# Kernel tuning notes

Measured on AMD Instinct MI355X. Metric: run time of the kernel, lower is better.

The kernel has to match this reference:

```python
import jax, jax.numpy as jnp
import numpy as np

N = 400_000   # active voxels
C = 128       # inplanes = outplanes
K = 9         # nplanes*3*3 kernel offsets (nplanes=1)
EPS = 1e-4    # scn BatchNormalization default eps


def setup_inputs() -> dict:
    key = jax.random.key(0)
    ks = jax.random.split(key, 5)
    feat = jax.random.normal(ks[0], (N, C), dtype=jnp.float32)
    # rulebook: neighbor active-site index per kernel offset, plus validity mask
    nbr_idx = jax.random.randint(ks[1], (N, K), 0, N, dtype=jnp.int32)
    nbr_idx = nbr_idx.at[:, K // 2].set(jnp.arange(N, dtype=jnp.int32))  # center = self
    nbr_mask = jax.random.uniform(ks[2], (N, K)) < 0.6
    nbr_mask = nbr_mask.at[:, K // 2].set(True)
    scale = 1.0 / np.sqrt(K * C)
    W1 = jax.random.normal(ks[3], (K, C, C), dtype=jnp.float32) * scale
    W2 = jax.random.normal(ks[4], (K, C, C), dtype=jnp.float32) * scale
    gamma1 = jnp.ones((C,), jnp.float32)
    beta1 = jnp.zeros((C,), jnp.float32)
    gamma2 = jnp.ones((C,), jnp.float32)
    beta2 = jnp.zeros((C,), jnp.float32)
    return {"feat": feat, "W1": W1, "W2": W2,
            "gamma1": gamma1, "beta1": beta1,
            "gamma2": gamma2, "beta2": beta2,
            "nbr_idx": nbr_idx, "nbr_mask": nbr_mask}


def _subm_conv(feat, nbr_idx, nbr_mask, W):
    # rulebook gather -> GEMM -> accumulate; output lives at the same active sites
    out = jnp.zeros((feat.shape[0], W.shape[2]), feat.dtype)
    for k in range(W.shape[0]):  # small fixed K=9 structural loop
        xk = jnp.where(nbr_mask[:, k:k + 1], feat[nbr_idx[:, k]], 0.0)
        out = out + xk @ W[k]
    return out


def _batchnorm(x, gamma, beta):
    mu = jnp.mean(x, axis=0)
    var = jnp.mean(jnp.square(x - mu), axis=0)
    return (x - mu) * (gamma * jax.lax.rsqrt(var + EPS)) + beta


def reference(feat, W1, W2, gamma1, beta1, gamma2, beta2, nbr_idx, nbr_mask):
    residual = feat                                   # scn.Identity (stride=1)
    out = _subm_conv(feat, nbr_idx, nbr_mask, W1)     # conv1
    out = jax.nn.relu(_batchnorm(out, gamma1, beta1))  # BatchNormReLU
    out = _subm_conv(out, nbr_idx, nbr_mask, W2)      # conv2
    out = _batchnorm(out, gamma2, beta2)              # bn2
    return jax.nn.relu(out + residual)                # AddTable + ReLU
```

## Files before the change

kernel.cpp:

```cpp
#include <hip/hip_runtime.h>


#define C_CH 128
#define K_OFF 9
#define MTILE 64

typedef __attribute__((ext_vector_type(8))) short bf16x8;
typedef __attribute__((ext_vector_type(4))) float f32x4;
typedef __attribute__((ext_vector_type(8))) unsigned short u16x8;

typedef __attribute__((address_space(1))) const unsigned int* gas_p;
typedef __attribute__((address_space(3))) unsigned int* las_p;

__device__ __forceinline__ void gload_lds16(const unsigned short* g, unsigned short* l) {
    __builtin_amdgcn_global_load_lds((gas_p)g, (las_p)l, 16, 0, 0);
}

__device__ __forceinline__ unsigned short f2b(float f) {
    union { float f; unsigned u; } v; v.f = f;
    unsigned r = v.u + 0x7fffu + ((v.u >> 16) & 1u);
    return (unsigned short)(r >> 16);
}
__device__ __forceinline__ float b2f(unsigned short h) {
    union { unsigned u; float f; } v; v.u = ((unsigned)h) << 16;
    return v.f;
}


__global__ void init_k(float* stats, unsigned int* zrow1, unsigned int* zrow2) {
    int t = threadIdx.x;
    if (t < 512) stats[t] = 0.f;
    if (t >= 512 && t < 514) ((int*)stats)[1024 + (t - 512)] = 0;
    if (t < 64) { zrow1[t] = 0u; zrow2[t] = 0u; }
}

__global__ void detect_mask_k(const unsigned char* __restrict__ m, int* flagA, int* flagB) {
    int i = blockIdx.x * blockDim.x + threadIdx.x;
    unsigned char v = m[i];
    if ((i & 3) != 0 && v != 0) atomicOr(flagA, 1);
    if (v > 1) atomicOr(flagB, 1);
}

__global__ void fold_idx_k(const int* __restrict__ nidx, const void* __restrict__ m,
                           const int* __restrict__ flagA, const int* __restrict__ flagB,
                           int* __restrict__ eidx, int n, int N) {
    int i = blockIdx.x * blockDim.x + threadIdx.x;
    if (i >= n) return;
    int fa = *flagA, fb = *flagB;
    bool t;
    if (!fa)       t = ((const int*)m)[i] != 0;
    else if (fb)   t = ((const unsigned*)m)[i] != 0;
    else           t = ((const unsigned char*)m)[i] != 0;
    eidx[i] = t ? nidx[i] : N;
}

__global__ void convert_feat_k(const float* __restrict__ x, unsigned short* __restrict__ y, int n4) {
    int i = blockIdx.x * blockDim.x + threadIdx.x;
    int s = gridDim.x * blockDim.x;
    for (; i < n4; i += s) {
        float4 f = ((const float4*)x)[i];
        ushort4 o;
        o.x = f2b(f.x); o.y = f2b(f.y); o.z = f2b(f.z); o.w = f2b(f.w);
        ((ushort4*)y)[i] = o;
    }
}

__global__ void pack_w_k(const float* __restrict__ W, unsigned short* __restrict__ Wp) {
    int i = blockIdx.x * blockDim.x + threadIdx.x;
    if (i >= K_OFF * 8 * 4 * 512) return;
    int j = i & 7;
    int l = (i >> 3) & 63;
    int frag = i >> 9;
    int ks = frag & 3;
    int nt = (frag >> 2) & 7;
    int ko = frag >> 5;
    int cin = ks * 32 + (l >> 4) * 8 + j;
    int cout = nt * 16 + (l & 15);
    Wp[i] = f2b(W[ko * C_CH * C_CH + cin * C_CH + cout]);
}


__global__ __launch_bounds__(256) void conv_kernel(
    const unsigned short* __restrict__ Xb,
    const unsigned short* __restrict__ Wp,
    const int* __restrict__ eidx,
    unsigned short* __restrict__ Yraw,
    float* __restrict__ statS, float* __restrict__ statQ)
{
    const int tid = threadIdx.x;
    const int lane = tid & 63;
    const int wv = tid >> 6;
    const int tile = blockIdx.x * MTILE;
    const int asub = lane >> 4;
    const int l15 = lane & 15;

    __shared__ alignas(16) unsigned short At[2][MTILE * C_CH];
    __shared__ int sIdxT[K_OFF][MTILE];

    for (int i = tid; i < MTILE * K_OFF; i += 256) {
        int r = i / K_OFF, k = i - r * K_OFF;
        sIdxT[k][r] = eidx[(size_t)(tile + r) * K_OFF + k];
    }
    __syncthreads();

    const int r_st = tid >> 4;
    const int ch_st = tid & 15;

    #define STAGE(buf, ko)                                                        \
        {                                                                         \
            _Pragma("unroll")                                                     \
            for (int jr = 0; jr < 4; ++jr) {                                      \
                int r = jr * 16 + r_st;                                           \
                int g = sIdxT[ko][r];                                             \
                const unsigned short* src =                                       \
                    Xb + (size_t)g * C_CH + ((ch_st ^ (r & 7)) * 8);              \
                unsigned short* dst = &At[buf][r * C_CH + ch_st * 8];             \
                gload_lds16(src, dst);                                            \
            }                                                                     \
        }

    f32x4 acc[4][2];
    #pragma unroll
    for (int m = 0; m < 4; ++m) { acc[m][0] = (f32x4){0,0,0,0}; acc[m][1] = (f32x4){0,0,0,0}; }

    STAGE(0, 0);
    __syncthreads();

    for (int ko = 0; ko < K_OFF; ++ko) {
        const int cur = ko & 1;

        bf16x8 bfrag[2][4];
        const unsigned short* wb = Wp + (size_t)ko * (8 * 4 * 512) + lane * 8;
        #pragma unroll
        for (int j = 0; j < 2; ++j)
            #pragma unroll
            for (int ks = 0; ks < 4; ++ks)
                bfrag[j][ks] = *(const bf16x8*)(wb + ((wv * 2 + j) * 4 + ks) * 512);

        if (ko < K_OFF - 1) STAGE(cur ^ 1, ko + 1);

        #pragma unroll
        for (int m = 0; m < 4; ++m) {
            bf16x8 a[4];
            #pragma unroll
            for (int ks = 0; ks < 4; ++ks) {
                int row = m * 16 + l15;
                int sc = (ks * 4 + asub) ^ (row & 7);
                a[ks] = *(const bf16x8*)((const char*)At[cur] + row * 256 + sc * 16);
            }
            #pragma unroll
            for (int ks = 0; ks < 4; ++ks) {
                acc[m][0] = __builtin_amdgcn_mfma_f32_16x16x32_bf16(a[ks], bfrag[0][ks], acc[m][0], 0, 0, 0);
                acc[m][1] = __builtin_amdgcn_mfma_f32_16x16x32_bf16(a[ks], bfrag[1][ks], acc[m][1], 0, 0, 0);
            }
        }
        __syncthreads();
    }
    #undef STAGE

    #pragma unroll
    for (int j = 0; j < 2; ++j) {
        float s = 0.f, q = 0.f;
        #pragma unroll
        for (int m = 0; m < 4; ++m)
            #pragma unroll
            for (int r = 0; r < 4; ++r) { float v = acc[m][j][r]; s += v; q += v * v; }
        s += __shfl_xor(s, 16); s += __shfl_xor(s, 32);
        q += __shfl_xor(q, 16); q += __shfl_xor(q, 32);
        if (lane < 16) {
            atomicAdd(&statS[wv * 32 + j * 16 + lane], s);
            atomicAdd(&statQ[wv * 32 + j * 16 + lane], q);
        }
    }

    #pragma unroll
    for (int m = 0; m < 4; ++m)
        #pragma unroll
        for (int j = 0; j < 2; ++j) {
            int col = (wv * 2 + j) * 16 + l15;
            #pragma unroll
            for (int r = 0; r < 4; ++r) {
                int row = tile + m * 16 + asub * 4 + r;
                Yraw[(size_t)row * C_CH + col] = f2b(acc[m][j][r]);
            }
        }
}


__global__ void finalize_bn_k(const float* __restrict__ S, const float* __restrict__ Q,
                              const float* __restrict__ gamma, const float* __restrict__ beta,
                              float* __restrict__ scale, float* __restrict__ bias, float invN) {
    int c = threadIdx.x;
    if (c < C_CH) {
        float mu = S[c] * invN;
        float var = Q[c] * invN - mu * mu;
        float inv = rsqrtf(var + 1e-4f);
        float sc = gamma[c] * inv;
        scale[c] = sc;
        bias[c] = beta[c] - mu * sc;
    }
}

__global__ void bn_relu_k(unsigned short* __restrict__ y,
                          const float* __restrict__ scale, const float* __restrict__ bias, int n8) {
    int i0 = blockIdx.x * blockDim.x + threadIdx.x;
    int S = gridDim.x * blockDim.x;
    int c0 = (i0 * 8) & (C_CH - 1);
    float sc[8], bs[8];
    #pragma unroll
    for (int j = 0; j < 8; ++j) { sc[j] = scale[c0 + j]; bs[j] = bias[c0 + j]; }
    for (int i = i0; i < n8; i += S) {
        u16x8 v = ((const u16x8*)y)[i];
        #pragma unroll
        for (int j = 0; j < 8; ++j) {
            float x = b2f((unsigned short)v[j]);
            x = fmaxf(x * sc[j] + bs[j], 0.f);
            v[j] = (short)f2b(x);
        }
        ((u16x8*)y)[i] = v;
    }
}

__global__ void final_fuse_k(const unsigned short* __restrict__ raw,
                             const float* __restrict__ feat,
                             const float* __restrict__ scale, const float* __restrict__ bias,
                             float* __restrict__ out, int n4) {
    int i0 = blockIdx.x * blockDim.x + threadIdx.x;
    int S = gridDim.x * blockDim.x;
    int c0 = (i0 * 4) & (C_CH - 1);
    float sc[4], bs[4];
    #pragma unroll
    for (int j = 0; j < 4; ++j) { sc[j] = scale[c0 + j]; bs[j] = bias[c0 + j]; }
    for (int i = i0; i < n4; i += S) {
        ushort4 r = ((const ushort4*)raw)[i];
        float4 f = ((const float4*)feat)[i];
        float4 o;
        o.x = fmaxf(b2f(r.x) * sc[0] + bs[0] + f.x, 0.f);
        o.y = fmaxf(b2f(r.y) * sc[1] + bs[1] + f.y, 0.f);
        o.z = fmaxf(b2f(r.z) * sc[2] + bs[2] + f.z, 0.f);
        o.w = fmaxf(b2f(r.w) * sc[3] + bs[3] + f.w, 0.f);
        ((float4*)out)[i] = o;
    }
}


extern "C" void kernel_launch(void* const* d_in, const int* in_sizes, int n_in,
                              void* d_out, int out_size, void* d_ws, size_t ws_size,
                              hipStream_t stream) {
    const float* feat = (const float*)d_in[0];
    const float* W1 = (const float*)d_in[1];
    const float* W2 = (const float*)d_in[2];
    const float* g1 = (const float*)d_in[3];
    const float* b1 = (const float*)d_in[4];
    const float* g2 = (const float*)d_in[5];
    const float* b2 = (const float*)d_in[6];
    const int* nidx = (const int*)d_in[7];
    const void* nmask = d_in[8];

    const int N = in_sizes[0] / C_CH;
    const int NK = N * K_OFF;

    char* ws = (char*)d_ws;
    unsigned short* featb = (unsigned short*)ws;
    size_t off = (size_t)(N + 1) * C_CH * 2;
    off = (off + 255) & ~(size_t)255;
    unsigned short* Wp1 = (unsigned short*)(ws + off); off += (size_t)K_OFF * C_CH * C_CH * 2;
    unsigned short* Wp2 = (unsigned short*)(ws + off); off += (size_t)K_OFF * C_CH * C_CH * 2;
    float* stats = (float*)(ws + off);
    float* S1 = stats;        float* Q1 = stats + 128;
    float* S2 = stats + 256;  float* Q2 = stats + 384;
    float* sc1 = stats + 512; float* bi1 = stats + 640;
    float* sc2 = stats + 768; float* bi2 = stats + 896;
    int* flagA = ((int*)stats) + 1024;
    int* flagB = ((int*)stats) + 1025;

    unsigned short* y1 = (unsigned short*)d_out;
    int* eidx = (int*)((char*)d_out + (size_t)134217728);
    unsigned short* out2raw = featb;

    hipLaunchKernelGGL(init_k, dim3(1), dim3(514), 0, stream,
                       stats, (unsigned int*)(featb + (size_t)N * C_CH),
                       (unsigned int*)(y1 + (size_t)N * C_CH));
    hipLaunchKernelGGL(detect_mask_k, dim3(64), dim3(256), 0, stream,
                       (const unsigned char*)nmask, flagA, flagB);
    hipLaunchKernelGGL(convert_feat_k, dim3(2048), dim3(256), 0, stream, feat, featb, N * C_CH / 4);
    hipLaunchKernelGGL(pack_w_k, dim3(576), dim3(256), 0, stream, W1, Wp1);
    hipLaunchKernelGGL(pack_w_k, dim3(576), dim3(256), 0, stream, W2, Wp2);
    hipLaunchKernelGGL(fold_idx_k, dim3((NK + 255) / 256), dim3(256), 0, stream,
                       nidx, nmask, flagA, flagB, eidx, NK, N);

    hipLaunchKernelGGL(conv_kernel, dim3(N / MTILE), dim3(256), 0, stream,
                       featb, Wp1, eidx, y1, S1, Q1);
    hipLaunchKernelGGL(finalize_bn_k, dim3(1), dim3(128), 0, stream, S1, Q1, g1, b1, sc1, bi1, 1.0f / N);
    hipLaunchKernelGGL(bn_relu_k, dim3(2048), dim3(256), 0, stream, y1, sc1, bi1, N * C_CH / 8);

    hipLaunchKernelGGL(conv_kernel, dim3(N / MTILE), dim3(256), 0, stream,
                       y1, Wp2, eidx, out2raw, S2, Q2);
    hipLaunchKernelGGL(finalize_bn_k, dim3(1), dim3(128), 0, stream, S2, Q2, g2, b2, sc2, bi2, 1.0f / N);
    hipLaunchKernelGGL(final_fuse_k, dim3(2048), dim3(256), 0, stream,
                       out2raw, feat, sc2, bi2, (float*)d_out, N * C_CH / 4);
}
```

Before: 590.1 us.

## Triple-buffer gathered rows with manual vmcnt waits and one barrier per offset

The conv kernel now uses three LDS buffers and prefetches two kernel offsets ahead instead of one. It replaces the per-iteration __syncthreads with explicit s_waitcnt vmcnt counts plus a single s_barrier, fully unrolling the 9-offset loop. The goal is to hide the latency of the random row gathers behind more MFMA work. The two weight-packing launches are also merged into one. This raises LDS use per block (about 48KB), which may lower occupancy, and the hand-tuned vmcnt counts are fragile if the compiler reorders loads.

```diff
diff --git a/kernel.cpp b/kernel.cpp
--- a/kernel.cpp
+++ b/kernel.cpp
@@ -65,18 +65,23 @@
     }
 }
 
-__global__ void pack_w_k(const float* __restrict__ W, unsigned short* __restrict__ Wp) {
+__global__ void pack_w_k(const float* __restrict__ W1, unsigned short* __restrict__ Wp1,
+                         const float* __restrict__ W2, unsigned short* __restrict__ Wp2) {
     int i = blockIdx.x * blockDim.x + threadIdx.x;
-    if (i >= K_OFF * 8 * 4 * 512) return;
-    int j = i & 7;
-    int l = (i >> 3) & 63;
-    int frag = i >> 9;
+    const int tot = K_OFF * 8 * 4 * 512;
+    const float* W = (i < tot) ? W1 : W2;
+    unsigned short* Wp = (i < tot) ? Wp1 : Wp2;
+    int ii = (i < tot) ? i : i - tot;
+    if (i >= 2 * tot) return;
+    int j = ii & 7;
+    int l = (ii >> 3) & 63;
+    int frag = ii >> 9;
     int ks = frag & 3;
     int nt = (frag >> 2) & 7;
     int ko = frag >> 5;
     int cin = ks * 32 + (l >> 4) * 8 + j;
     int cout = nt * 16 + (l & 15);
-    Wp[i] = f2b(W[ko * C_CH * C_CH + cin * C_CH + cout]);
+    Wp[ii] = f2b(W[ko * C_CH * C_CH + cin * C_CH + cout]);
 }
 
 
@@ -94,7 +99,7 @@
     const int asub = lane >> 4;
     const int l15 = lane & 15;
 
-    __shared__ alignas(16) unsigned short At[2][MTILE * C_CH];
+    __shared__ alignas(16) unsigned short At[3][MTILE * C_CH];
     __shared__ int sIdxT[K_OFF][MTILE];
 
     for (int i = tid; i < MTILE * K_OFF; i += 256) {
@@ -124,38 +129,49 @@
     for (int m = 0; m < 4; ++m) { acc[m][0] = (f32x4){0,0,0,0}; acc[m][1] = (f32x4){0,0,0,0}; }
 
     STAGE(0, 0);
-    __syncthreads();
-
-    for (int ko = 0; ko < K_OFF; ++ko) {
-        const int cur = ko & 1;
-
-        bf16x8 bfrag[2][4];
-        const unsigned short* wb = Wp + (size_t)ko * (8 * 4 * 512) + lane * 8;
-        #pragma unroll
-        for (int j = 0; j < 2; ++j)
-            #pragma unroll
-            for (int ks = 0; ks < 4; ++ks)
-                bfrag[j][ks] = *(const bf16x8*)(wb + ((wv * 2 + j) * 4 + ks) * 512);
-
-        if (ko < K_OFF - 1) STAGE(cur ^ 1, ko + 1);
-
-        #pragma unroll
-        for (int m = 0; m < 4; ++m) {
-            bf16x8 a[4];
-            #pragma unroll
-            for (int ks = 0; ks < 4; ++ks) {
-                int row = m * 16 + l15;
-                int sc = (ks * 4 + asub) ^ (row & 7);
-                a[ks] = *(const bf16x8*)((const char*)At[cur] + row * 256 + sc * 16);
-            }
-            #pragma unroll
-            for (int ks = 0; ks < 4; ++ks) {
-                acc[m][0] = __builtin_amdgcn_mfma_f32_16x16x32_bf16(a[ks], bfrag[0][ks], acc[m][0], 0, 0, 0);
-                acc[m][1] = __builtin_amdgcn_mfma_f32_16x16x32_bf16(a[ks], bfrag[1][ks], acc[m][1], 0, 0, 0);
-            }
-        }
-        __syncthreads();
-    }
+    STAGE(1, 1);
+
+    #define CONV_ITER(KO, VM)                                                     \
+        {                                                                         \
+            bf16x8 bfrag0[4], bfrag1[4];                                          \
+            const unsigned short* wb = Wp + (size_t)(KO) * (8 * 4 * 512) + lane * 8; \
+            _Pragma("unroll")                                                     \
+            for (int ks = 0; ks < 4; ++ks) {                                      \
+                bfrag0[ks] = *(const bf16x8*)(wb + ((wv * 2 + 0) * 4 + ks) * 512);\
+                bfrag1[ks] = *(const bf16x8*)(wb + ((wv * 2 + 1) * 4 + ks) * 512);\
+            }                                                                     \
+            __builtin_amdgcn_sched_barrier(0);                                    \
+            asm volatile("s_waitcnt vmcnt(" #VM ")" ::: "memory");                \
+            __builtin_amdgcn_s_barrier();                                         \
+            __builtin_amdgcn_sched_barrier(0);                                    \
+            if ((KO) + 2 < K_OFF) { STAGE((((KO) + 2) % 3), (KO) + 2); }          \
+            _Pragma("unroll")                                                     \
+            for (int m = 0; m < 4; ++m) {                                         \
+                bf16x8 a[4];                                                      \
+                _Pragma("unroll")                                                 \
+                for (int ks = 0; ks < 4; ++ks) {                                  \
+                    int row = m * 16 + l15;                                       \
+                    int sc = (ks * 4 + asub) ^ (row & 7);                         \
+                    a[ks] = *(const bf16x8*)((const char*)At[(KO) % 3] + row * 256 + sc * 16); \
+                }                                                                 \
+                _Pragma("unroll")                                                 \
+                for (int ks = 0; ks < 4; ++ks) {                                  \
+                    acc[m][0] = __builtin_amdgcn_mfma_f32_16x16x32_bf16(a[ks], bfrag0[ks], acc[m][0], 0, 0, 0); \
+                    acc[m][1] = __builtin_amdgcn_mfma_f32_16x16x32_bf16(a[ks], bfrag1[ks], acc[m][1], 0, 0, 0); \
+                }                                                                 \
+            }                                                                     \
+        }
+
+    CONV_ITER(0, 12)
+    CONV_ITER(1, 20)
+    CONV_ITER(2, 20)
+    CONV_ITER(3, 20)
+    CONV_ITER(4, 20)
+    CONV_ITER(5, 20)
+    CONV_ITER(6, 20)
+    CONV_ITER(7, 20)
+    CONV_ITER(8, 16)
+    #undef CONV_ITER
     #undef STAGE
 
     #pragma unroll
@@ -284,8 +300,7 @@
     hipLaunchKernelGGL(detect_mask_k, dim3(64), dim3(256), 0, stream,
                        (const unsigned char*)nmask, flagA, flagB);
     hipLaunchKernelGGL(convert_feat_k, dim3(2048), dim3(256), 0, stream, feat, featb, N * C_CH / 4);
-    hipLaunchKernelGGL(pack_w_k, dim3(576), dim3(256), 0, stream, W1, Wp1);
-    hipLaunchKernelGGL(pack_w_k, dim3(576), dim3(256), 0, stream, W2, Wp2);
+    hipLaunchKernelGGL(pack_w_k, dim3(1152), dim3(256), 0, stream, W1, Wp1, W2, Wp2);
     hipLaunchKernelGGL(fold_idx_k, dim3((NK + 255) / 256), dim3(256), 0, stream,
                        nidx, nmask, flagA, flagB, eidx, NK, N);
 
```

New measurement: 574.3 us. 2.7% less time.
